# Kernel optimization log

Hardware: AMD Instinct MI355X
Metric: run time of the kernel (lower is better)

The kernel has to match this reference:

```python
import jax, jax.numpy as jnp
import numpy as np

DIM = 64          # head_dim (per-head embedding dim)
MAX_GRID = 64     # max_grid_size
BASE = 10000.0    # RoPE base


def setup_inputs() -> dict:
    key = jax.random.key(0)
    k1, _ = jax.random.split(key)
    B, S, H, D = 32, 1024, 16, DIM
    x = jax.random.normal(k1, (B, S, H, D), dtype=jnp.float32)
    # Per-sample (rows, cols) with rows*cols == S, exercising the ragged path.
    grids = [(32, 32), (16, 64), (64, 16), (32, 32)]
    gs = np.array([grids[b % len(grids)] for b in range(B)], dtype=np.int32)
    grid_sizes = jnp.asarray(gs)
    return {"x": x, "grid_sizes": grid_sizes}


def _rope2d(x, grid_sizes):
    b, s, h, d = x.shape
    half = d // 2
    # theta: [half]
    theta = 1.0 / BASE ** (jnp.arange(0, d, 2, dtype=jnp.float32) / d)
    # cos/sin caches over positions 0..MAX_GRID-1: [MAX_GRID, half]
    ang = jnp.arange(MAX_GRID, dtype=jnp.float32)[:, None] * theta
    cache_cos, cache_sin = jnp.cos(ang), jnp.sin(ang)

    # flat position -> (row, col) per sample, using per-sample col count
    cols = grid_sizes[:, 1].astype(jnp.int32)          # [b]
    p = jnp.arange(s, dtype=jnp.int32)                 # [s]
    i = p[None, :] // cols[:, None]                    # [b, s] row index
    j = p[None, :] % cols[:, None]                     # [b, s] col index

    # gather rotation terms, broadcast over heads: [b, s, 1, half]
    cos_r = cache_cos[i][:, :, None, :]
    sin_r = cache_sin[i][:, :, None, :]
    cos_c = cache_cos[j][:, :, None, :]
    sin_c = cache_sin[j][:, :, None, :]

    xr = x.reshape(b, s, h, half, 2)
    x0, x1 = xr[..., 0], xr[..., 1]
    # row rotation
    y0 = x0 * cos_r - x1 * sin_r
    y1 = x1 * cos_r + x0 * sin_r
    # col rotation (applied to the row-rotated values, as in the original)
    z0 = y0 * cos_c - y1 * sin_c
    z1 = y1 * cos_c + y0 * sin_c
    return jnp.stack([z0, z1], axis=-1).reshape(b, s, h, d)


def reference(x, grid_sizes):
    return _rope2d(x, grid_sizes)
```

## Files before the change

### kernel.cpp

```cpp
#include <hip/hip_runtime.h>
#include <math.h>


#define S_LOG2 10
#define H_LOG2 4
#define D_LOG2 6

__global__ __launch_bounds__(256) void rope2d_kernel(
    const float4* __restrict__ x,
    const int* __restrict__ grid_sizes,
    float4* __restrict__ out,
    int n4)
{
    int g = blockIdx.x * 256 + threadIdx.x;
    if (g >= n4) return;

    int e    = g << 2;
    int k    = (e & ((1 << D_LOG2) - 1)) >> 1;
    int bs   = e >> (D_LOG2 + H_LOG2);
    int s    = bs & ((1 << S_LOG2) - 1);
    int b    = bs >> S_LOG2;

    int cols = grid_sizes[2 * b + 1];
    int i    = s / cols;
    int j    = s - i * cols;
    float ij = (float)(i + j);

    const float C       = -0.41524101186092029f;
    const float INV_2PI = 0.15915494309189535f;

    float t0 = __builtin_amdgcn_exp2f((float)k * C);
    float t1 = __builtin_amdgcn_exp2f((float)(k + 1) * C);

    float r0 = ij * t0 * INV_2PI;  r0 -= floorf(r0);
    float r1 = ij * t1 * INV_2PI;  r1 -= floorf(r1);

    float s0 = __builtin_amdgcn_sinf(r0);
    float c0 = __builtin_amdgcn_cosf(r0);
    float s1 = __builtin_amdgcn_sinf(r1);
    float c1 = __builtin_amdgcn_cosf(r1);

    float4 v = x[g];
    float4 o;
    o.x = v.x * c0 - v.y * s0;
    o.y = v.y * c0 + v.x * s0;
    o.z = v.z * c1 - v.w * s1;
    o.w = v.w * c1 + v.z * s1;
    out[g] = o;
}

extern "C" void kernel_launch(void* const* d_in, const int* in_sizes, int n_in,
                              void* d_out, int out_size, void* d_ws, size_t ws_size,
                              hipStream_t stream) {
    const float4* x  = (const float4*)d_in[0];
    const int*    gs = (const int*)d_in[1];
    float4*       o  = (float4*)d_out;

    int n4 = in_sizes[0] >> 2;
    int blocks = (n4 + 255) / 256;

    rope2d_kernel<<<blocks, 256, 0, stream>>>(x, gs, o, n4);
}
```

Measured before the change: 221.8 us.

## Process four float4 chunks per thread with nontemporal loads and stores

Each thread now handles four float4 vectors, one 256-element chunk per (b,s) row, instead of one. All four loads are issued up front to raise memory-level parallelism, and the theta exponentials are hoisted so they are computed once per thread. Loads and stores use nontemporal hints to avoid polluting the cache on this streaming workload. The bounds check is removed and the grid is sized as n4/(256*4), which assumes the element count divides evenly.

```diff
diff --git a/kernel.cpp b/kernel.cpp
--- a/kernel.cpp
+++ b/kernel.cpp
@@ -2,62 +2,68 @@
 #include <math.h>
 
 
-#define S_LOG2 10
-#define H_LOG2 4
-#define D_LOG2 6
+typedef float vfloat4 __attribute__((ext_vector_type(4)));
+
+#define CHUNKS 4
 
 __global__ __launch_bounds__(256) void rope2d_kernel(
-    const float4* __restrict__ x,
+    const vfloat4* __restrict__ x,
     const int* __restrict__ grid_sizes,
-    float4* __restrict__ out,
-    int n4)
+    vfloat4* __restrict__ out)
 {
-    int g = blockIdx.x * 256 + threadIdx.x;
-    if (g >= n4) return;
+    const int tid   = threadIdx.x;
+    const int base4 = blockIdx.x * (256 * CHUNKS);
+    const int bs0   = blockIdx.x * CHUNKS;
 
-    int e    = g << 2;
-    int k    = (e & ((1 << D_LOG2) - 1)) >> 1;
-    int bs   = e >> (D_LOG2 + H_LOG2);
-    int s    = bs & ((1 << S_LOG2) - 1);
-    int b    = bs >> S_LOG2;
-
-    int cols = grid_sizes[2 * b + 1];
-    int i    = s / cols;
-    int j    = s - i * cols;
-    float ij = (float)(i + j);
+    const int k = (tid & 15) << 1;
 
     const float C       = -0.41524101186092029f;
     const float INV_2PI = 0.15915494309189535f;
 
-    float t0 = __builtin_amdgcn_exp2f((float)k * C);
-    float t1 = __builtin_amdgcn_exp2f((float)(k + 1) * C);
+    const float t0 = __builtin_amdgcn_exp2f((float)k * C);
+    const float t1 = __builtin_amdgcn_exp2f((float)(k + 1) * C);
 
-    float r0 = ij * t0 * INV_2PI;  r0 -= floorf(r0);
-    float r1 = ij * t1 * INV_2PI;  r1 -= floorf(r1);
+    vfloat4 v[CHUNKS];
+#pragma unroll
+    for (int c = 0; c < CHUNKS; ++c)
+        v[c] = __builtin_nontemporal_load(&x[base4 + c * 256 + tid]);
 
-    float s0 = __builtin_amdgcn_sinf(r0);
-    float c0 = __builtin_amdgcn_cosf(r0);
-    float s1 = __builtin_amdgcn_sinf(r1);
-    float c1 = __builtin_amdgcn_cosf(r1);
+#pragma unroll
+    for (int c = 0; c < CHUNKS; ++c) {
+        const int bs   = bs0 + c;
+        const int s    = bs & 1023;
+        const int b    = bs >> 10;
+        const int cols = grid_sizes[2 * b + 1];
+        const int i    = s / cols;
+        const int j    = s - i * cols;
+        const float ij = (float)(i + j);
 
-    float4 v = x[g];
-    float4 o;
-    o.x = v.x * c0 - v.y * s0;
-    o.y = v.y * c0 + v.x * s0;
-    o.z = v.z * c1 - v.w * s1;
-    o.w = v.w * c1 + v.z * s1;
-    out[g] = o;
+        float r0 = ij * t0 * INV_2PI;  r0 -= floorf(r0);
+        float r1 = ij * t1 * INV_2PI;  r1 -= floorf(r1);
+
+        const float s0 = __builtin_amdgcn_sinf(r0);
+        const float c0 = __builtin_amdgcn_cosf(r0);
+        const float s1 = __builtin_amdgcn_sinf(r1);
+        const float c1 = __builtin_amdgcn_cosf(r1);
+
+        vfloat4 o;
+        o.x = v[c].x * c0 - v[c].y * s0;
+        o.y = v[c].y * c0 + v[c].x * s0;
+        o.z = v[c].z * c1 - v[c].w * s1;
+        o.w = v[c].w * c1 + v[c].z * s1;
+        __builtin_nontemporal_store(o, &out[base4 + c * 256 + tid]);
+    }
 }
 
 extern "C" void kernel_launch(void* const* d_in, const int* in_sizes, int n_in,
                               void* d_out, int out_size, void* d_ws, size_t ws_size,
                               hipStream_t stream) {
-    const float4* x  = (const float4*)d_in[0];
-    const int*    gs = (const int*)d_in[1];
-    float4*       o  = (float4*)d_out;
+    const vfloat4* x  = (const vfloat4*)d_in[0];
+    const int*     gs = (const int*)d_in[1];
+    vfloat4*       o  = (vfloat4*)d_out;
 
-    int n4 = in_sizes[0] >> 2;
-    int blocks = (n4 + 255) / 256;
+    const int n4     = in_sizes[0] >> 2;
+    const int blocks = n4 / (256 * CHUNKS);
 
-    rope2d_kernel<<<blocks, 256, 0, stream>>>(x, gs, o, n4);
+    rope2d_kernel<<<blocks, 256, 0, stream>>>(x, gs, o);
 }
```

After: 218.0 us. Within noise of the previous version (-1.7%).
